# Kernel tuning notes

Hardware: AMD Instinct MI355X
Metric: run time of the kernel (lower is better)

## Reference

```python
import jax, jax.numpy as jnp
import numpy as np

N = 100000   # nodes
E = 1600000  # edges
D = 64       # in/hidden channels
C = 40       # out channels (classes)
L = 5        # n_layers


def setup_inputs() -> dict:
    key = jax.random.key(0)
    ks = jax.random.split(key, 8)
    x = jax.random.normal(ks[0], (N, D), dtype=jnp.float32)
    edge_src = jax.random.randint(ks[1], (E,), 0, N)
    edge_dst = jax.random.randint(ks[2], (E,), 0, N)
    edge_weight = jax.random.uniform(ks[3], (E,), dtype=jnp.float32)
    # learned params: 4 hidden convs (64->64) stacked, 1 output conv (64->40)
    W = jax.random.normal(ks[4], (L - 1, D, D), dtype=jnp.float32) / np.sqrt(D)
    b = jax.random.normal(ks[5], (L - 1, D), dtype=jnp.float32) * 0.01
    W_out = jax.random.normal(ks[6], (D, C), dtype=jnp.float32) / np.sqrt(D)
    b_out = jax.random.normal(ks[7], (C,), dtype=jnp.float32) * 0.01
    return {"x": x, "edge_weight": edge_weight, "W": W, "b": b,
            "W_out": W_out, "b_out": b_out,
            "edge_src": edge_src, "edge_dst": edge_dst}


def _gcn_conv(x, W, b, src, dst, w):
    # GCNConv: A_norm @ (x @ W) + b, with A_norm given as an edge list
    h = x @ W                          # [N, out]
    msg = h[src] * w[:, None]          # [E, out] gather + edge scaling
    agg = jax.ops.segment_sum(msg, dst, num_segments=N)  # scatter-add
    return agg + b


def reference(x, edge_weight, W, b, W_out, b_out, edge_src, edge_dst):
    # layers 0..3: conv -> relu (dropout inactive in eval mode)
    for i in range(L - 1):
        x = jax.nn.relu(_gcn_conv(x, W[i], b[i], edge_src, edge_dst, edge_weight))
    # last layer: conv only (no act/dropout after final layer)
    x = _gcn_conv(x, W_out, b_out, edge_src, edge_dst, edge_weight)
    return x  # [N, C]
```

## Files before the change

### kernel.cpp

```cpp
#include <hip/hip_runtime.h>
#include <hip/hip_fp16.h>

#define N_NODES 100000
#define E_EDGES 1600000
#define E4 (E_EDGES / 4)
#define NBUCKETS ((N_NODES + 127) / 128)
#define CHUNK 8192
#define NCHUNK ((E_EDGES + CHUNK - 1) / CHUNK)
#define HM (NBUCKETS * NCHUNK)
#define NSB ((HM + 1023) / 1024)

template<int DOUT, bool RELU_IN>
__global__ __launch_bounds__(256) void gemm_tile(const float* __restrict__ X,
                                                 const float* __restrict__ W,
                                                 __half* __restrict__ H) {
    __shared__ float Xs[64][68];
    __shared__ float Ws[64 * DOUT];
    const int tid = threadIdx.x;

    for (int i = tid; i < 64 * DOUT / 4; i += 256) {
        reinterpret_cast<float4*>(Ws)[i] = reinterpret_cast<const float4*>(W)[i];
    }

    const int row0 = blockIdx.x * 64;
#pragma unroll
    for (int p = 0; p < 4; ++p) {
        int idx = p * 256 + tid;
        int r = idx >> 4;
        int c = (idx & 15) << 2;
        float4 v = make_float4(0.f, 0.f, 0.f, 0.f);
        if (row0 + r < N_NODES) {
            v = *reinterpret_cast<const float4*>(X + (size_t)(row0 + r) * 64 + c);
        }
        if (RELU_IN) {
            v.x = fmaxf(v.x, 0.f); v.y = fmaxf(v.y, 0.f);
            v.z = fmaxf(v.z, 0.f); v.w = fmaxf(v.w, 0.f);
        }
        *reinterpret_cast<float4*>(&Xs[r][c]) = v;
    }
    __syncthreads();

    const int tr = (tid >> 4) << 2;
    const int tc = (tid & 15) << 2;
    if (tc < DOUT) {
        float acc[4][4];
#pragma unroll
        for (int i = 0; i < 4; ++i)
#pragma unroll
            for (int j = 0; j < 4; ++j) acc[i][j] = 0.f;

#pragma unroll 8
        for (int k = 0; k < 64; ++k) {
            float4 wv = *reinterpret_cast<const float4*>(&Ws[k * DOUT + tc]);
            float xv[4];
#pragma unroll
            for (int i = 0; i < 4; ++i) xv[i] = Xs[tr + i][k];
#pragma unroll
            for (int i = 0; i < 4; ++i) {
                acc[i][0] += xv[i] * wv.x;
                acc[i][1] += xv[i] * wv.y;
                acc[i][2] += xv[i] * wv.z;
                acc[i][3] += xv[i] * wv.w;
            }
        }
#pragma unroll
        for (int i = 0; i < 4; ++i) {
            int r = row0 + tr + i;
            if (r < N_NODES) {
                union { __half2 h2[2]; uint2 u; } pk;
                pk.h2[0] = __halves2half2(__float2half(acc[i][0]), __float2half(acc[i][1]));
                pk.h2[1] = __halves2half2(__float2half(acc[i][2]), __float2half(acc[i][3]));
                *reinterpret_cast<uint2*>(H + (size_t)r * DOUT + tc) = pk.u;
            }
        }
    }
}

__global__ __launch_bounds__(256) void chunk_hist(const int4* __restrict__ dst4,
                                                  int* __restrict__ histM) {
    __shared__ int lh[NBUCKETS];
    const int tid = threadIdx.x, c = blockIdx.x;
    for (int i = tid; i < NBUCKETS; i += 256) lh[i] = 0;
    __syncthreads();
    const int q0 = c * (CHUNK / 4);
    for (int q = tid; q < CHUNK / 4; q += 256) {
        if (q0 + q < E4) {
            int4 d = dst4[q0 + q];
            atomicAdd(&lh[d.x >> 7], 1);
            atomicAdd(&lh[d.y >> 7], 1);
            atomicAdd(&lh[d.z >> 7], 1);
            atomicAdd(&lh[d.w >> 7], 1);
        }
    }
    __syncthreads();
    for (int i = tid; i < NBUCKETS; i += 256) histM[i * NCHUNK + c] = lh[i];
}

__global__ __launch_bounds__(256) void scan_blocks(const int* __restrict__ in,
                                                   int* __restrict__ out,
                                                   int* __restrict__ bsums) {
    __shared__ int wsum[4];
    const int tid = threadIdx.x, lane = tid & 63, wv = tid >> 6;
    const int base = blockIdx.x * 1024 + tid * 4;
    int v[4];
    int s = 0;
#pragma unroll
    for (int j = 0; j < 4; ++j) {
        v[j] = (base + j < HM) ? in[base + j] : 0;
        s += v[j];
    }
    int inc = s;
#pragma unroll
    for (int o = 1; o < 64; o <<= 1) {
        int t = __shfl_up(inc, o, 64);
        if (lane >= o) inc += t;
    }
    if (lane == 63) wsum[wv] = inc;
    __syncthreads();
    int woff = 0;
    for (int w2 = 0; w2 < wv; ++w2) woff += wsum[w2];
    int run = woff + inc - s;
#pragma unroll
    for (int j = 0; j < 4; ++j) {
        if (base + j < HM) out[base + j] = run;
        run += v[j];
    }
    if (tid == 255) bsums[blockIdx.x] = woff + inc;
}

__global__ __launch_bounds__(256) void scan_mid256(const int* __restrict__ bs,
                                                   int* __restrict__ boff) {
    __shared__ int wsum[4];
    const int tid = threadIdx.x, lane = tid & 63, wv = tid >> 6;
    int v = (tid < NSB) ? bs[tid] : 0;
    int inc = v;
#pragma unroll
    for (int o = 1; o < 64; o <<= 1) {
        int t = __shfl_up(inc, o, 64);
        if (lane >= o) inc += t;
    }
    if (lane == 63) wsum[wv] = inc;
    __syncthreads();
    int woff = 0;
    for (int w2 = 0; w2 < wv; ++w2) woff += wsum[w2];
    if (tid < NSB) boff[tid] = woff + inc - v;
}

__global__ __launch_bounds__(256) void scan_add(int* __restrict__ out,
                                                const int* __restrict__ boff) {
    const int base = blockIdx.x * 1024 + threadIdx.x * 4;
    const int a = boff[blockIdx.x];
#pragma unroll
    for (int j = 0; j < 4; ++j) {
        if (base + j < HM) out[base + j] += a;
    }
}

__global__ __launch_bounds__(256) void chunk_scatter(const int4* __restrict__ src4,
                                                     const int4* __restrict__ dst4,
                                                     const float4* __restrict__ ew4,
                                                     const int* __restrict__ hs,
                                                     int2* __restrict__ tmp) {
    __shared__ int lcur[NBUCKETS];
    const int tid = threadIdx.x, c = blockIdx.x;
    for (int i = tid; i < NBUCKETS; i += 256) lcur[i] = hs[i * NCHUNK + c];
    __syncthreads();
    const int q0 = c * (CHUNK / 4);
    for (int q = tid; q < CHUNK / 4; q += 256) {
        if (q0 + q < E4) {
            int4 s = src4[q0 + q];
            int4 d = dst4[q0 + q];
            float4 w = ew4[q0 + q];
            int p0 = atomicAdd(&lcur[d.x >> 7], 1);
            tmp[p0] = make_int2(s.x | ((d.x & 127) << 17), __float_as_int(w.x));
            int p1 = atomicAdd(&lcur[d.y >> 7], 1);
            tmp[p1] = make_int2(s.y | ((d.y & 127) << 17), __float_as_int(w.y));
            int p2 = atomicAdd(&lcur[d.z >> 7], 1);
            tmp[p2] = make_int2(s.z | ((d.z & 127) << 17), __float_as_int(w.z));
            int p3 = atomicAdd(&lcur[d.w >> 7], 1);
            tmp[p3] = make_int2(s.w | ((d.w & 127) << 17), __float_as_int(w.w));
        }
    }
}

__global__ __launch_bounds__(256) void build_csr(const int2* __restrict__ tmp,
                                                 const int* __restrict__ hs,
                                                 int* __restrict__ off,
                                                 int2* __restrict__ csr) {
    __shared__ int lhist[128];
    __shared__ int lcur[128];
    __shared__ int wtot[4];
    const int b = blockIdx.x;
    const int tid = threadIdx.x, lane = tid & 63, wv = tid >> 6;
    const int base = hs[b * NCHUNK];
    const int end  = (b + 1 < NBUCKETS) ? hs[(b + 1) * NCHUNK] : E_EDGES;

    if (tid < 128) lhist[tid] = 0;
    __syncthreads();

    for (int e = base + tid; e < end; e += 256) {
        int dl = (tmp[e].x >> 17) & 127;
        atomicAdd(&lhist[dl], 1);
    }
    __syncthreads();

    int v = (tid < 128) ? lhist[tid] : 0;
    int inc = v;
#pragma unroll
    for (int o = 1; o < 64; o <<= 1) {
        int t = __shfl_up(inc, o, 64);
        if (lane >= o) inc += t;
    }
    if (lane == 63) wtot[wv] = inc;
    __syncthreads();
    if (tid < 128) {
        int excl = inc - v + ((wv == 1) ? wtot[0] : 0);
        lcur[tid] = base + excl;
        int node = b * 128 + tid;
        if (node < N_NODES) off[node] = base + excl;
    }
    if (b == NBUCKETS - 1 && tid == 0) off[N_NODES] = E_EDGES;
    __syncthreads();

    for (int e = base + tid; e < end; e += 256) {
        int2 t2 = tmp[e];
        int dl = (t2.x >> 17) & 127;
        int p = atomicAdd(&lcur[dl], 1);
        csr[p] = make_int2(t2.x & 0x1FFFF, t2.y);
    }
}

template<int DOUT>
__global__ __launch_bounds__(256) void aggregate(const __half* __restrict__ H,
                                                 const int* __restrict__ off,
                                                 const int2* __restrict__ csr,
                                                 const float* __restrict__ bvec,
                                                 float* __restrict__ AGG) {
    const int node = (int)((blockIdx.x * 256 + threadIdx.x) >> 6);
    const int lane = threadIdx.x & 63;
    if (node >= N_NODES) return;
    const int k0 = __builtin_amdgcn_readfirstlane(off[node]);
    const int k1 = __builtin_amdgcn_readfirstlane(off[node + 1]);
    const bool active = (DOUT == 64) || (lane < DOUT);
    float acc = active ? bvec[lane] : 0.f;
    int k = k0;
    for (; k + 3 < k1; k += 4) {
        int2 e0 = csr[k], e1 = csr[k + 1], e2 = csr[k + 2], e3 = csr[k + 3];
        int s0 = __builtin_amdgcn_readfirstlane(e0.x);
        int s1 = __builtin_amdgcn_readfirstlane(e1.x);
        int s2 = __builtin_amdgcn_readfirstlane(e2.x);
        int s3 = __builtin_amdgcn_readfirstlane(e3.x);
        float h0 = 0.f, h1 = 0.f, h2 = 0.f, h3 = 0.f;
        if (active) {
            h0 = __half2float(H[(size_t)s0 * DOUT + lane]);
            h1 = __half2float(H[(size_t)s1 * DOUT + lane]);
            h2 = __half2float(H[(size_t)s2 * DOUT + lane]);
            h3 = __half2float(H[(size_t)s3 * DOUT + lane]);
        }
        acc += h0 * __int_as_float(e0.y) + h1 * __int_as_float(e1.y)
             + h2 * __int_as_float(e2.y) + h3 * __int_as_float(e3.y);
    }
    for (; k < k1; ++k) {
        int2 e0 = csr[k];
        int s0 = __builtin_amdgcn_readfirstlane(e0.x);
        if (active) acc += __half2float(H[(size_t)s0 * DOUT + lane]) * __int_as_float(e0.y);
    }
    if (active) AGG[(size_t)node * DOUT + lane] = acc;
}

extern "C" void kernel_launch(void* const* d_in, const int* in_sizes, int n_in,
                              void* d_out, int out_size, void* d_ws, size_t ws_size,
                              hipStream_t stream) {
    const float* x    = (const float*)d_in[0];
    const float* ew   = (const float*)d_in[1];
    const float* W    = (const float*)d_in[2];
    const float* b    = (const float*)d_in[3];
    const float* Wout = (const float*)d_in[4];
    const float* bout = (const float*)d_in[5];
    const int*   src  = (const int*)d_in[6];
    const int*   dst  = (const int*)d_in[7];
    float* out = (float*)d_out;

    char* wsp = (char*)d_ws;
    __half* H2  = (__half*)wsp;
    int2*   tmp = (int2*)wsp;
    size_t  o   = (size_t)N_NODES * 64 * sizeof(__half);
    float*  AGG = (float*)(wsp + o); o += (size_t)N_NODES * 64 * sizeof(float);
    int2*   csr = (int2*)(wsp + o);  o += (size_t)E_EDGES * sizeof(int2);
    int*    off = (int*)(wsp + o);   o += (size_t)(N_NODES + 1) * sizeof(int);
    int*  histM = (int*)(wsp + o);   o += (size_t)HM * sizeof(int);
    int*    hs  = (int*)(wsp + o);   o += (size_t)HM * sizeof(int);
    int*  bsums = (int*)(wsp + o);   o += (size_t)NSB * sizeof(int);
    int*   boff = (int*)(wsp + o);   o += (size_t)NSB * sizeof(int);

    dim3 blk(256);
    const int gemmGrid = (N_NODES + 63) / 64;
    const int aggGrid  = (N_NODES * 64 + 255) / 256;

    chunk_hist<<<NCHUNK, blk, 0, stream>>>((const int4*)dst, histM);
    scan_blocks<<<NSB, blk, 0, stream>>>(histM, hs, bsums);
    scan_mid256<<<1, blk, 0, stream>>>(bsums, boff);
    scan_add<<<NSB, blk, 0, stream>>>(hs, boff);
    chunk_scatter<<<NCHUNK, blk, 0, stream>>>((const int4*)src, (const int4*)dst,
                                              (const float4*)ew, hs, tmp);
    build_csr<<<NBUCKETS, blk, 0, stream>>>(tmp, hs, off, csr);

    gemm_tile<64, false><<<gemmGrid, blk, 0, stream>>>(x, W, H2);
    aggregate<64><<<aggGrid, blk, 0, stream>>>(H2, off, csr, b, AGG);

    for (int i = 1; i < 4; ++i) {
        gemm_tile<64, true><<<gemmGrid, blk, 0, stream>>>(AGG, W + (size_t)i * 64 * 64, H2);
        aggregate<64><<<aggGrid, blk, 0, stream>>>(H2, off, csr, b + (size_t)i * 64, AGG);
    }

    gemm_tile<40, true><<<gemmGrid, blk, 0, stream>>>(AGG, Wout, H2);
    aggregate<40><<<aggGrid, blk, 0, stream>>>(H2, off, csr, bout, out);
}
```

Measured before the change: 383.6 us.

## Fuse aggregation with next layer's GEMM and unroll edge loop by eight

```diff
diff --git a/kernel.cpp b/kernel.cpp
--- a/kernel.cpp
+++ b/kernel.cpp
@@ -10,7 +10,50 @@
 #define HM (NBUCKETS * NCHUNK)
 #define NSB ((HM + 1023) / 1024)
 
-template<int DOUT, bool RELU_IN>
+template<int HSTRIDE>
+__device__ __forceinline__ float agg_edges(const __half* __restrict__ Hin,
+                                           const int2* __restrict__ csr,
+                                           int k0, int k1, int lane, bool active,
+                                           float acc) {
+    int k = k0;
+    for (; k + 7 < k1; k += 8) {
+        int2 e[8];
+#pragma unroll
+        for (int u = 0; u < 8; ++u) e[u] = csr[k + u];
+        float h[8];
+#pragma unroll
+        for (int u = 0; u < 8; ++u) {
+            int s = __builtin_amdgcn_readfirstlane(e[u].x);
+            h[u] = active ? __half2float(Hin[(size_t)s * HSTRIDE + lane]) : 0.f;
+        }
+#pragma unroll
+        for (int u = 0; u < 8; ++u) acc += h[u] * __int_as_float(e[u].y);
+    }
+    for (; k + 3 < k1; k += 4) {
+        int2 e0 = csr[k], e1 = csr[k + 1], e2 = csr[k + 2], e3 = csr[k + 3];
+        int s0 = __builtin_amdgcn_readfirstlane(e0.x);
+        int s1 = __builtin_amdgcn_readfirstlane(e1.x);
+        int s2 = __builtin_amdgcn_readfirstlane(e2.x);
+        int s3 = __builtin_amdgcn_readfirstlane(e3.x);
+        float h0 = 0.f, h1 = 0.f, h2 = 0.f, h3 = 0.f;
+        if (active) {
+            h0 = __half2float(Hin[(size_t)s0 * HSTRIDE + lane]);
+            h1 = __half2float(Hin[(size_t)s1 * HSTRIDE + lane]);
+            h2 = __half2float(Hin[(size_t)s2 * HSTRIDE + lane]);
+            h3 = __half2float(Hin[(size_t)s3 * HSTRIDE + lane]);
+        }
+        acc += h0 * __int_as_float(e0.y) + h1 * __int_as_float(e1.y)
+             + h2 * __int_as_float(e2.y) + h3 * __int_as_float(e3.y);
+    }
+    for (; k < k1; ++k) {
+        int2 e0 = csr[k];
+        int s0 = __builtin_amdgcn_readfirstlane(e0.x);
+        if (active) acc += __half2float(Hin[(size_t)s0 * HSTRIDE + lane]) * __int_as_float(e0.y);
+    }
+    return acc;
+}
+
+template<int DOUT>
 __global__ __launch_bounds__(256) void gemm_tile(const float* __restrict__ X,
                                                  const float* __restrict__ W,
                                                  __half* __restrict__ H) {
@@ -31,10 +74,6 @@
         float4 v = make_float4(0.f, 0.f, 0.f, 0.f);
         if (row0 + r < N_NODES) {
             v = *reinterpret_cast<const float4*>(X + (size_t)(row0 + r) * 64 + c);
-        }
-        if (RELU_IN) {
-            v.x = fmaxf(v.x, 0.f); v.y = fmaxf(v.y, 0.f);
-            v.z = fmaxf(v.z, 0.f); v.w = fmaxf(v.w, 0.f);
         }
         *reinterpret_cast<float4*>(&Xs[r][c]) = v;
     }
@@ -74,6 +113,92 @@
             }
         }
     }
+}
+
+template<int DOUT>
+__global__ __launch_bounds__(512) void fused_agg_gemm(const __half* __restrict__ Hin,
+                                                      const int* __restrict__ off,
+                                                      const int2* __restrict__ csr,
+                                                      const float* __restrict__ bprev,
+                                                      const float* __restrict__ W,
+                                                      __half* __restrict__ Hout) {
+    __shared__ float Xs[128][68];
+    __shared__ float Ws[64 * DOUT];
+    const int tid = threadIdx.x;
+    const int lane = tid & 63;
+    const int wv = tid >> 6;
+    const int row0 = blockIdx.x * 128;
+
+    for (int i = tid; i < 64 * DOUT / 4; i += 512) {
+        reinterpret_cast<float4*>(Ws)[i] = reinterpret_cast<const float4*>(W)[i];
+    }
+
+    const float bias = bprev[lane];
+
+#pragma unroll 1
+    for (int it = 0; it < 16; ++it) {
+        const int nodeIdx = wv + it * 8;
+        const int node = row0 + nodeIdx;
+        if (node < N_NODES) {
+            const int k0 = __builtin_amdgcn_readfirstlane(off[node]);
+            const int k1 = __builtin_amdgcn_readfirstlane(off[node + 1]);
+            float acc = agg_edges<64>(Hin, csr, k0, k1, lane, true, bias);
+            Xs[nodeIdx][lane] = fmaxf(acc, 0.f);
+        }
+    }
+    __syncthreads();
+
+    const int tr = (tid >> 4) << 2;
+    const int tc = (tid & 15) << 2;
+    if (tc < DOUT) {
+        float acc[4][4];
+#pragma unroll
+        for (int i = 0; i < 4; ++i)
+#pragma unroll
+            for (int j = 0; j < 4; ++j) acc[i][j] = 0.f;
+
+#pragma unroll 8
+        for (int k = 0; k < 64; ++k) {
+            float4 wvv = *reinterpret_cast<const float4*>(&Ws[k * DOUT + tc]);
+            float xv[4];
+#pragma unroll
+            for (int i = 0; i < 4; ++i) xv[i] = Xs[tr + i][k];
+#pragma unroll
+            for (int i = 0; i < 4; ++i) {
+                acc[i][0] += xv[i] * wvv.x;
+                acc[i][1] += xv[i] * wvv.y;
+                acc[i][2] += xv[i] * wvv.z;
+                acc[i][3] += xv[i] * wvv.w;
+            }
+        }
+#pragma unroll
+        for (int i = 0; i < 4; ++i) {
+            int r = row0 + tr + i;
+            if (r < N_NODES) {
+                union { __half2 h2[2]; uint2 u; } pk;
+                pk.h2[0] = __halves2half2(__float2half(acc[i][0]), __float2half(acc[i][1]));
+                pk.h2[1] = __halves2half2(__float2half(acc[i][2]), __float2half(acc[i][3]));
+                *reinterpret_cast<uint2*>(Hout + (size_t)r * DOUT + tc) = pk.u;
+            }
+        }
+    }
+}
+
+template<int DOUT>
+__global__ __launch_bounds__(256) void aggregate(const __half* __restrict__ H,
+                                                 const int* __restrict__ off,
+                                                 const int2* __restrict__ csr,
+                                                 const float* __restrict__ bvec,
+                                                 float* __restrict__ AGG) {
+    const int node = (int)((blockIdx.x * 256 + threadIdx.x) >> 6);
+    const int lane = threadIdx.x & 63;
+    if (node >= N_NODES) return;
+    const int k0 = __builtin_amdgcn_readfirstlane(off[node]);
+    const int k1 = __builtin_amdgcn_readfirstlane(off[node + 1]);
+    const bool active = (DOUT == 64) || (lane < DOUT);
+    float acc = active ? bvec[lane] : 0.f;
+    acc = agg_edges<DOUT>(H, csr, k0, k1, lane, active, acc);
+    if (active) AGG[(size_t)node * DOUT + lane] = acc;
 }
 
 __global__ __launch_bounds__(256) void chunk_hist(const int4* __restrict__ dst4,
@@ -230,44 +355,6 @@
     }
 }
 
-template<int DOUT>
-__global__ __launch_bounds__(256) void aggregate(const __half* __restrict__ H,
-                                                 const int* __restrict__ off,
-                                                 const int2* __restrict__ csr,
-                                                 const float* __restrict__ bvec,
-                                                 float* __restrict__ AGG) {
-    const int node = (int)((blockIdx.x * 256 + threadIdx.x) >> 6);
-    const int lane = threadIdx.x & 63;
-    if (node >= N_NODES) return;
-    const int k0 = __builtin_amdgcn_readfirstlane(off[node]);
-    const int k1 = __builtin_amdgcn_readfirstlane(off[node + 1]);
-    const bool active = (DOUT == 64) || (lane < DOUT);
-    float acc = active ? bvec[lane] : 0.f;
-    int k = k0;
-    for (; k + 3 < k1; k += 4) {
-        int2 e0 = csr[k], e1 = csr[k + 1], e2 = csr[k + 2], e3 = csr[k + 3];
-        int s0 = __builtin_amdgcn_readfirstlane(e0.x);
-        int s1 = __builtin_amdgcn_readfirstlane(e1.x);
-        int s2 = __builtin_amdgcn_readfirstlane(e2.x);
-        int s3 = __builtin_amdgcn_readfirstlane(e3.x);
-        float h0 = 0.f, h1 = 0.f, h2 = 0.f, h3 = 0.f;
-        if (active) {
-            h0 = __half2float(H[(size_t)s0 * DOUT + lane]);
-            h1 = __half2float(H[(size_t)s1 * DOUT + lane]);
-            h2 = __half2float(H[(size_t)s2 * DOUT + lane]);
-            h3 = __half2float(H[(size_t)s3 * DOUT + lane]);
-        }
-        acc += h0 * __int_as_float(e0.y) + h1 * __int_as_float(e1.y)
-             + h2 * __int_as_float(e2.y) + h3 * __int_as_float(e3.y);
-    }
-    for (; k < k1; ++k) {
-        int2 e0 = csr[k];
-        int s0 = __builtin_amdgcn_readfirstlane(e0.x);
-        if (active) acc += __half2float(H[(size_t)s0 * DOUT + lane]) * __int_as_float(e0.y);
-    }
-    if (active) AGG[(size_t)node * DOUT + lane] = acc;
-}
-
 extern "C" void kernel_launch(void* const* d_in, const int* in_sizes, int n_in,
                               void* d_out, int out_size, void* d_ws, size_t ws_size,
                               hipStream_t stream) {
@@ -282,20 +369,21 @@
     float* out = (float*)d_out;
 
     char* wsp = (char*)d_ws;
-    __half* H2  = (__half*)wsp;
-    int2*   tmp = (int2*)wsp;
-    size_t  o   = (size_t)N_NODES * 64 * sizeof(__half);
-    float*  AGG = (float*)(wsp + o); o += (size_t)N_NODES * 64 * sizeof(float);
-    int2*   csr = (int2*)(wsp + o);  o += (size_t)E_EDGES * sizeof(int2);
-    int*    off = (int*)(wsp + o);   o += (size_t)(N_NODES + 1) * sizeof(int);
-    int*  histM = (int*)(wsp + o);   o += (size_t)HM * sizeof(int);
-    int*    hs  = (int*)(wsp + o);   o += (size_t)HM * sizeof(int);
-    int*  bsums = (int*)(wsp + o);   o += (size_t)NSB * sizeof(int);
-    int*   boff = (int*)(wsp + o);   o += (size_t)NSB * sizeof(int);
+    size_t  o   = 0;
+    __half* HA  = (__half*)(wsp + o); o += (size_t)N_NODES * 64 * sizeof(__half);
+    __half* HB  = (__half*)(wsp + o); o += (size_t)N_NODES * 64 * sizeof(__half);
+    int2*   csr = (int2*)(wsp + o);   o += (size_t)E_EDGES * sizeof(int2);
+    int2*   tmp = (int2*)(wsp + o);   o += (size_t)E_EDGES * sizeof(int2);
+    int*    off = (int*)(wsp + o);    o += (size_t)(N_NODES + 1) * sizeof(int);
+    int*  histM = (int*)(wsp + o);    o += (size_t)HM * sizeof(int);
+    int*    hs  = (int*)(wsp + o);    o += (size_t)HM * sizeof(int);
+    int*  bsums = (int*)(wsp + o);    o += (size_t)NSB * sizeof(int);
+    int*   boff = (int*)(wsp + o);    o += (size_t)NSB * sizeof(int);
 
     dim3 blk(256);
-    const int gemmGrid = (N_NODES + 63) / 64;
-    const int aggGrid  = (N_NODES * 64 + 255) / 256;
+    const int gemmGrid  = (N_NODES + 63) / 64;
+    const int fusedGrid = (N_NODES + 127) / 128;
+    const int aggGrid   = (N_NODES * 64 + 255) / 256;
 
     chunk_hist<<<NCHUNK, blk, 0, stream>>>((const int4*)dst, histM);
     scan_blocks<<<NSB, blk, 0, stream>>>(histM, hs, bsums);
@@ -305,14 +393,12 @@
                                               (const float4*)ew, hs, tmp);
     build_csr<<<NBUCKETS, blk, 0, stream>>>(tmp, hs, off, csr);
 
-    gemm_tile<64, false><<<gemmGrid, blk, 0, stream>>>(x, W, H2);
-    aggregate<64><<<aggGrid, blk, 0, stream>>>(H2, off, csr, b, AGG);
-
-    for (int i = 1; i < 4; ++i) {
-        gemm_tile<64, true><<<gemmGrid, blk, 0, stream>>>(AGG, W + (size_t)i * 64 * 64, H2);
-        aggregate<64><<<aggGrid, blk, 0, stream>>>(H2, off, csr, b + (size_t)i * 64, AGG);
-    }
-
-    gemm_tile<40, true><<<gemmGrid, blk, 0, stream>>>(AGG, Wout, H2);
-    aggregate<40><<<aggGrid, blk, 0, stream>>>(H2, off, csr, bout, out);
-}
+    gemm_tile<64><<<gemmGrid, blk, 0, stream>>>(x, W, HA);
+
+    fused_agg_gemm<64><<<fusedGrid, 512, 0, stream>>>(HA, off, csr, b,          W + 1 * 4096, HB);
+    fused_agg_gemm<64><<<fusedGrid, 512, 0, stream>>>(HB, off, csr, b + 64,     W + 2 * 4096, HA);
+    fused_agg_gemm<64><<<fusedGrid, 512, 0, stream>>>(HA, off, csr, b + 128,    W + 3 * 4096, HB);
+    fused_agg_gemm<40><<<fusedGrid, 512, 0, stream>>>(HB, off, csr, b + 192,    Wout,         HA);
+
+    aggregate<40><<<aggGrid, blk, 0, stream>>>(HA, off, csr, bout, out);
+}
```

After: 471.0 us. 22.8% more time.

## Slice hidden features into 8-channel column blocks for cache-local aggregation

Applied to the files above, without the earlier changes.

```diff
diff --git a/kernel.cpp b/kernel.cpp
--- a/kernel.cpp
+++ b/kernel.cpp
@@ -10,7 +10,7 @@
 #define HM (NBUCKETS * NCHUNK)
 #define NSB ((HM + 1023) / 1024)
 
-template<int DOUT, bool RELU_IN>
+template<int DOUT, bool RELU_IN, bool SLICED>
 __global__ __launch_bounds__(256) void gemm_tile(const float* __restrict__ X,
                                                  const float* __restrict__ W,
                                                  __half* __restrict__ H) {
@@ -70,7 +70,12 @@
                 union { __half2 h2[2]; uint2 u; } pk;
                 pk.h2[0] = __halves2half2(__float2half(acc[i][0]), __float2half(acc[i][1]));
                 pk.h2[1] = __halves2half2(__float2half(acc[i][2]), __float2half(acc[i][3]));
-                *reinterpret_cast<uint2*>(H + (size_t)r * DOUT + tc) = pk.u;
+                if (SLICED) {
+                    __half* p = H + ((size_t)(tc >> 3) * N_NODES + (size_t)r) * 8 + (tc & 7);
+                    *reinterpret_cast<uint2*>(p) = pk.u;
+                } else {
+                    *reinterpret_cast<uint2*>(H + (size_t)r * DOUT + tc) = pk.u;
+                }
             }
         }
     }
@@ -227,6 +232,50 @@
         int dl = (t2.x >> 17) & 127;
         int p = atomicAdd(&lcur[dl], 1);
         csr[p] = make_int2(t2.x & 0x1FFFF, t2.y);
+    }
+}
+
+__global__ __launch_bounds__(256) void aggregate_sliced(const __half* __restrict__ Hs,
+                                                        const int* __restrict__ off,
+                                                        const int2* __restrict__ csr,
+                                                        const float* __restrict__ bvec,
+                                                        float* __restrict__ AGG) {
+    const int bid = blockIdx.x;
+    const int slice = bid & 7;
+    const int chunk = bid >> 3;
+    const int tid = threadIdx.x, lane = tid & 63, wv = tid >> 6;
+    const int e  = lane >> 2;
+    const int cp = lane & 3;
+    const float b0 = bvec[slice * 8 + cp * 2];
+    const float b1 = bvec[slice * 8 + cp * 2 + 1];
+    const __half* Hbase = Hs + (size_t)slice * N_NODES * 8 + cp * 2;
+
+#pragma unroll 1
+    for (int i = 0; i < 4; ++i) {
+        const int node = chunk * 16 + wv * 4 + i;
+        if (node >= N_NODES) return;
+        const int k0 = __builtin_amdgcn_readfirstlane(off[node]);
+        const int k1 = __builtin_amdgcn_readfirstlane(off[node + 1]);
+        float ax = 0.f, ay = 0.f;
+        for (int t = k0; t < k1; t += 16) {
+            const int idx = t + e;
+            const bool vld = idx < k1;
+            int2 ec = csr[vld ? idx : k0];
+            const float w = vld ? __int_as_float(ec.y) : 0.f;
+            float2 hf = __half22float2(
+                *reinterpret_cast<const __half2*>(Hbase + (size_t)ec.x * 8));
+            ax += hf.x * w;
+            ay += hf.y * w;
+        }
+#pragma unroll
+        for (int o2 = 4; o2 < 64; o2 <<= 1) {
+            ax += __shfl_xor(ax, o2);
+            ay += __shfl_xor(ay, o2);
+        }
+        if (lane < 4) {
+            *reinterpret_cast<float2*>(AGG + (size_t)node * 64 + slice * 8 + cp * 2) =
+                make_float2(ax + b0, ay + b1);
+        }
     }
 }
 
@@ -296,6 +345,7 @@
     dim3 blk(256);
     const int gemmGrid = (N_NODES + 63) / 64;
     const int aggGrid  = (N_NODES * 64 + 255) / 256;
+    const int slicedGrid = 8 * ((N_NODES + 15) / 16);
 
     chunk_hist<<<NCHUNK, blk, 0, stream>>>((const int4*)dst, histM);
     scan_blocks<<<NSB, blk, 0, stream>>>(histM, hs, bsums);
@@ -305,14 +355,14 @@
                                               (const float4*)ew, hs, tmp);
     build_csr<<<NBUCKETS, blk, 0, stream>>>(tmp, hs, off, csr);
 
-    gemm_tile<64, false><<<gemmGrid, blk, 0, stream>>>(x, W, H2);
-    aggregate<64><<<aggGrid, blk, 0, stream>>>(H2, off, csr, b, AGG);
+    gemm_tile<64, false, true><<<gemmGrid, blk, 0, stream>>>(x, W, H2);
+    aggregate_sliced<<<slicedGrid, blk, 0, stream>>>(H2, off, csr, b, AGG);
 
     for (int i = 1; i < 4; ++i) {
-        gemm_tile<64, true><<<gemmGrid, blk, 0, stream>>>(AGG, W + (size_t)i * 64 * 64, H2);
-        aggregate<64><<<aggGrid, blk, 0, stream>>>(H2, off, csr, b + (size_t)i * 64, AGG);
-    }
-
-    gemm_tile<40, true><<<gemmGrid, blk, 0, stream>>>(AGG, Wout, H2);
+        gemm_tile<64, true, true><<<gemmGrid, blk, 0, stream>>>(AGG, W + (size_t)i * 64 * 64, H2);
+        aggregate_sliced<<<slicedGrid, blk, 0, stream>>>(H2, off, csr, b + (size_t)i * 64, AGG);
+    }
+
+    gemm_tile<40, true, false><<<gemmGrid, blk, 0, stream>>>(AGG, Wout, H2);
     aggregate<40><<<aggGrid, blk, 0, stream>>>(H2, off, csr, bout, out);
 }
```

Result: slower. 754.1 us (+96.6%).
